# Optimization experiments

Measured on AMD Instinct MI355X. Metric: run time of the kernel, lower is better.

Reference implementation:

```python
import jax, jax.numpy as jnp
import numpy as np

HEADS = 8
LOCAL_ATTN_CTX = 64  # local_attn_ctx
BLOCKSIZE = 32       # only used for divisibility assert in original


def _strided_transpose(x, local_attn_ctx):
    # [n, t, e] -> group seq into (bT_ctx, local) blocks and transpose them
    n, t, e = x.shape
    bT_ctx = t // local_attn_ctx
    x = x.reshape(n, bT_ctx, local_attn_ctx, e)
    x = jnp.transpose(x, (0, 2, 1, 3))
    return x.reshape(n, t, e)


def setup_inputs() -> dict:
    key = jax.random.key(0)
    kq, kk, kv = jax.random.split(key, 3)
    shape = (4, 4096, 512)  # [batch, n_ctx, embd]
    return {
        "q": jax.random.normal(kq, shape, dtype=jnp.float32),
        "k": jax.random.normal(kk, shape, dtype=jnp.float32),
        "v": jax.random.normal(kv, shape, dtype=jnp.float32),
    }


def reference(q, k, v):
    n_ctx = q.shape[1]
    bT_ctx = n_ctx // LOCAL_ATTN_CTX
    assert bT_ctx % BLOCKSIZE == 0
    # strided permutation of the sequence axis
    qs = _strided_transpose(q, LOCAL_ATTN_CTX)
    ks = _strided_transpose(k, LOCAL_ATTN_CTX)
    vs = _strided_transpose(v, LOCAL_ATTN_CTX)
    n_state = q.shape[-1] // HEADS
    scale = np.float32(1.0 / np.sqrt(n_state))
    # full attention over the permuted sequence (as in the torch impl)
    w = jnp.einsum('nte,nse->nts', qs, ks)          # [n, t, t]
    w = jax.nn.softmax(w * scale, axis=-1)
    a = jnp.einsum('nts,nse->nte', w, vs)           # [n, t, e]
    # inverse strided regrouping
    n, t, e = a.shape
    a = a.reshape(n, LOCAL_ATTN_CTX, bT_ctx, e)
    a = jnp.transpose(a, (0, 2, 1, 3))
    return a.reshape(n, t, e)
```

## Files before the change

### kernel.cpp

```cpp
#include <hip/hip_runtime.h>


typedef _Float16 half8 __attribute__((ext_vector_type(8)));
typedef float f32x16 __attribute__((ext_vector_type(16)));
typedef float f32x4v __attribute__((ext_vector_type(4)));

#define B 4
#define S 4096
#define D 512
#define QT 64
#define NT 64
#define NELEM (B * S * D)

#define QSCALE 0.18033688011112042f
#define M0 20.0f

__global__ __launch_bounds__(256) void cvt(const float* __restrict__ k,
                                           const float* __restrict__ v,
                                           _Float16* __restrict__ k16,
                                           _Float16* __restrict__ v16) {
  __shared__ half8 tile[32][65];
  const int tid = threadIdx.x;
  int bx = blockIdx.x;
  if (bx < 512) {
    const int b = bx >> 7;
    const int t0 = (bx & 127) * 32;
#pragma unroll
    for (int p = 0; p < 8; ++p) {
      const int tl = p * 4 + (tid >> 6);
      const int dcl = tid & 63;
      const float* src = k + ((size_t)(b * S + t0 + tl) * D) + dcl * 8;
      f32x4v x = *(const f32x4v*)src;
      f32x4v y = *(const f32x4v*)(src + 4);
      half8 h;
      h[0] = (_Float16)x[0]; h[1] = (_Float16)x[1]; h[2] = (_Float16)x[2]; h[3] = (_Float16)x[3];
      h[4] = (_Float16)y[0]; h[5] = (_Float16)y[1]; h[6] = (_Float16)y[2]; h[7] = (_Float16)y[3];
      tile[tl][dcl] = h;
    }
    __syncthreads();
#pragma unroll
    for (int p = 0; p < 8; ++p) {
      const int dcw = p * 8 + (tid >> 5);
      const int tw = tid & 31;
      ((half8*)k16)[(size_t)(b * 64 + dcw) * S + t0 + tw] = tile[tw][dcw];
    }
  } else {
    bx -= 512;
    const int i = bx * 256 + tid;
    const int dq = i & 127;
    const int bt8 = i >> 7;
    const int b = bt8 >> 9, t8 = bt8 & 511;
    const float* src = v + ((size_t)(b * S + t8 * 8) * D) + dq * 4;
    f32x4v r[8];
#pragma unroll
    for (int j = 0; j < 8; ++j) r[j] = *(const f32x4v*)(src + (size_t)j * D);
    half8* dst = (half8*)v16 + ((size_t)bt8 * 512 + dq * 4);
#pragma unroll
    for (int c = 0; c < 4; ++c) {
      half8 h;
#pragma unroll
      for (int j = 0; j < 8; ++j) h[j] = (_Float16)r[j][c];
      dst[c] = h;
    }
  }
}

#define PBUF_H 5120
#define PBUF_OFF 0
#define SRED_OFF (2 * PBUF_H * 2)
#define LBUF_OFF (SRED_OFF + 16384)
#define SMEM_SZ  (LBUF_OFF + 512)

__global__ __launch_bounds__(1024, 4)
__attribute__((amdgpu_waves_per_eu(4, 4)))
void attn(const float* __restrict__ q,
          const _Float16* __restrict__ k16,
          const _Float16* __restrict__ v16,
          float* __restrict__ out) {
  __shared__ __align__(16) char smem[SMEM_SZ];
  _Float16* Pbuf = (_Float16*)(smem + PBUF_OFF);
  float*    Sred = (float*)(smem + SRED_OFF);
  float*    Lbuf = (float*)(smem + LBUF_OFF);

  const int tid = threadIdx.x;
  const int w = tid >> 6, lane = tid & 63;
  const int m32 = lane & 31, hi = lane >> 5;

  const int bx = blockIdx.x;
  const int xc = bx & 7, rr0 = bx >> 3;
  const int b = xc >> 1;
  const int qt = ((xc & 1) << 5) + rr0;

  if (w < 8) {
    const int rg = w & 1, kh = (w >> 1) & 1, dh = (w >> 2) & 1;
    const int qrow0 = qt * QT + rg * 32;

    const _Float16* kb = k16 + ((size_t)(b * 64 + dh * 32 + hi) * S + kh * 32 + m32) * 8;
    half8 kg[2][2];
#pragma unroll
    for (int i = 0; i < 2; ++i)
      kg[0][i] = *(const half8*)(kb + (size_t)i * (S * 16));

    half8 qf[16];
    {
      const float* qb = q + ((size_t)(b * S + qrow0 + m32) * D) + dh * 256 + hi * 8;
#pragma unroll
      for (int ks = 0; ks < 16; ++ks) {
        f32x4v x = *(const f32x4v*)(qb + ks * 16);
        f32x4v y = *(const f32x4v*)(qb + ks * 16 + 4);
        half8 h;
        h[0] = (_Float16)(x[0] * QSCALE); h[1] = (_Float16)(x[1] * QSCALE);
        h[2] = (_Float16)(x[2] * QSCALE); h[3] = (_Float16)(x[3] * QSCALE);
        h[4] = (_Float16)(y[0] * QSCALE); h[5] = (_Float16)(y[1] * QSCALE);
        h[6] = (_Float16)(y[2] * QSCALE); h[7] = (_Float16)(y[3] * QSCALE);
        qf[ks] = h;
      }
    }
    float* sredq = Sred + (kh * 2 + rg) * 1024 + lane * 4;

    if (dh == 1) {
      for (int t = 0; t <= NT; ++t) {
        asm volatile("" ::: "memory");
        __builtin_amdgcn_s_barrier();
        asm volatile("" ::: "memory");
        if (t == NT) break;
        f32x16 sa = {};
#pragma unroll
        for (int g = 0; g < 8; ++g) {
          if (g < 7) {
#pragma unroll
            for (int i = 0; i < 2; ++i)
              kg[(g + 1) & 1][i] = *(const half8*)(kb + (size_t)((g + 1) * 2 + i) * (S * 16) +
                                                   (size_t)t * 512);
          } else if (t + 1 < NT) {
#pragma unroll
            for (int i = 0; i < 2; ++i)
              kg[0][i] = *(const half8*)(kb + (size_t)i * (S * 16) + (size_t)(t + 1) * 512);
          }
          __builtin_amdgcn_s_setprio(1);
          sa = __builtin_amdgcn_mfma_f32_32x32x16_f16(qf[g * 2], kg[g & 1][0], sa, 0, 0, 0);
          sa = __builtin_amdgcn_mfma_f32_32x32x16_f16(qf[g * 2 + 1], kg[g & 1][1], sa, 0, 0, 0);
          __builtin_amdgcn_s_setprio(0);
        }
#pragma unroll
        for (int rq = 0; rq < 4; ++rq) {
          f32x4v x = {sa[rq * 4 + 0], sa[rq * 4 + 1], sa[rq * 4 + 2], sa[rq * 4 + 3]};
          *(f32x4v*)(sredq + rq * 256) = x;
        }
        asm volatile("s_waitcnt lgkmcnt(0)" ::: "memory");
        __builtin_amdgcn_s_barrier();
        asm volatile("" ::: "memory");
      }
      asm volatile("" ::: "memory");
      __builtin_amdgcn_s_barrier();
    } else {
      float lacc[16];
#pragma unroll
      for (int r = 0; r < 16; ++r) lacc[r] = 0.f;

      for (int t = 0; t <= NT; ++t) {
        asm volatile("s_waitcnt lgkmcnt(0)" ::: "memory");
        __builtin_amdgcn_s_barrier();
        asm volatile("" ::: "memory");
        if (t == NT) break;
        f32x16 sa = {};
#pragma unroll
        for (int g = 0; g < 8; ++g) {
          if (g < 7) {
#pragma unroll
            for (int i = 0; i < 2; ++i)
              kg[(g + 1) & 1][i] = *(const half8*)(kb + (size_t)((g + 1) * 2 + i) * (S * 16) +
                                                   (size_t)t * 512);
          } else if (t + 1 < NT) {
#pragma unroll
            for (int i = 0; i < 2; ++i)
              kg[0][i] = *(const half8*)(kb + (size_t)i * (S * 16) + (size_t)(t + 1) * 512);
          }
          __builtin_amdgcn_s_setprio(1);
          sa = __builtin_amdgcn_mfma_f32_32x32x16_f16(qf[g * 2], kg[g & 1][0], sa, 0, 0, 0);
          sa = __builtin_amdgcn_mfma_f32_32x32x16_f16(qf[g * 2 + 1], kg[g & 1][1], sa, 0, 0, 0);
          __builtin_amdgcn_s_setprio(0);
        }
        asm volatile("" ::: "memory");
        __builtin_amdgcn_s_barrier();
        asm volatile("" ::: "memory");
        _Float16* pq = &Pbuf[(t & 1) * PBUF_H + (kh * 2 + rg) * 1280];
#pragma unroll
        for (int rq = 0; rq < 4; ++rq) {
          f32x4v x = *(const f32x4v*)(sredq + rq * 256);
#pragma unroll
          for (int c = 0; c < 4; ++c) {
            const int r = rq * 4 + c;
            float p = __builtin_amdgcn_exp2f(fminf((sa[r] + x[c]) - M0, 15.0f));
            lacc[r] += p;
            const int row = c + 8 * rq + 4 * hi;
            pq[row * 40 + m32] = (_Float16)p;
          }
        }
      }

#pragma unroll
      for (int r = 0; r < 16; ++r) {
        float vv = lacc[r];
        vv += __shfl_xor(vv, 1);  vv += __shfl_xor(vv, 2);
        vv += __shfl_xor(vv, 4);  vv += __shfl_xor(vv, 8);
        vv += __shfl_xor(vv, 16);
        lacc[r] = vv;
      }
      if (m32 == 0) {
#pragma unroll
        for (int r = 0; r < 16; ++r) {
          const int row = (r & 3) + 8 * (r >> 2) + 4 * hi;
          Lbuf[kh * 64 + rg * 32 + row] = lacc[r];
        }
      }
      asm volatile("s_waitcnt lgkmcnt(0)" ::: "memory");
      __builtin_amdgcn_s_barrier();
    }
  } else {
    const int j = w - 8;
    f32x16 o[2][2];
#pragma unroll
    for (int rt = 0; rt < 2; ++rt)
#pragma unroll
      for (int dn = 0; dn < 2; ++dn) o[rt][dn] = (f32x16){};

    half8 vf[2][2], pf[2][4];
    const _Float16* vb0 = v16 + ((size_t)(b * 512 + hi) * 512 + j * 64 + m32) * 8;
#pragma unroll
    for (int dn = 0; dn < 2; ++dn)
      vf[0][dn] = *(const half8*)(vb0 + dn * 256);

    for (int t = 0; t <= NT; ++t) {
      asm volatile("" ::: "memory");
      __builtin_amdgcn_s_barrier();
      asm volatile("" ::: "memory");
      if (t > 0) {
        const _Float16* pb = &Pbuf[((t - 1) & 1) * PBUF_H];
#pragma unroll
        for (int rt = 0; rt < 2; ++rt)
#pragma unroll
          for (int ks = 0; ks < 4; ++ks)
            pf[rt][ks] = *(const half8*)(pb + ((ks >> 1) * 2 + rt) * 1280 + m32 * 40 +
                                         (ks & 1) * 16 + hi * 8);
      }
      if (t < NT) {
        asm volatile("" ::: "memory");
        __builtin_amdgcn_s_barrier();
        asm volatile("" ::: "memory");
      }
      if (t > 0) {
        const int u = t - 1;
        const _Float16* vb = vb0 + (size_t)u * 32768;
#pragma unroll
        for (int ks = 0; ks < 4; ++ks) {
          if (ks < 3) {
#pragma unroll
            for (int dn = 0; dn < 2; ++dn)
              vf[(ks + 1) & 1][dn] = *(const half8*)(vb + (size_t)(ks + 1) * 8192 + dn * 256);
          } else if (u + 1 < NT) {
#pragma unroll
            for (int dn = 0; dn < 2; ++dn)
              vf[0][dn] = *(const half8*)(vb + (size_t)32768 + dn * 256);
          }
          __builtin_amdgcn_s_setprio(1);
#pragma unroll
          for (int rt = 0; rt < 2; ++rt)
#pragma unroll
            for (int dn = 0; dn < 2; ++dn)
              o[rt][dn] = __builtin_amdgcn_mfma_f32_32x32x16_f16(pf[rt][ks], vf[ks & 1][dn],
                                                                 o[rt][dn], 0, 0, 0);
          __builtin_amdgcn_s_setprio(0);
        }
      }
    }

    asm volatile("" ::: "memory");
    __builtin_amdgcn_s_barrier();
    asm volatile("" ::: "memory");
    float* ob = out + (size_t)(b * S + qt * QT) * D + j * 64;
#pragma unroll
    for (int rt = 0; rt < 2; ++rt)
#pragma unroll
      for (int r = 0; r < 16; ++r) {
        const int row = rt * 32 + (r & 3) + 8 * (r >> 2) + 4 * hi;
        const float lt = Lbuf[row] + Lbuf[64 + row];
        const float inv = 1.0f / lt;
#pragma unroll
        for (int dn = 0; dn < 2; ++dn)
          ob[(size_t)row * D + dn * 32 + m32] = o[rt][dn][r] * inv;
      }
  }
}

extern "C" void kernel_launch(void* const* d_in, const int* in_sizes, int n_in,
                              void* d_out, int out_size, void* d_ws, size_t ws_size,
                              hipStream_t stream) {
  const float* q = (const float*)d_in[0];
  const float* k = (const float*)d_in[1];
  const float* v = (const float*)d_in[2];
  float* out = (float*)d_out;

  _Float16* k16 = (_Float16*)d_ws;
  _Float16* v16 = k16 + NELEM;

  cvt<<<1536, 256, 0, stream>>>(k, v, k16, v16);
  attn<<<256, 1024, 0, stream>>>(q, k16, v16, out);
}
```

Measured before the change: 300.5 us.

## Stage shared K tiles in LDS via async global-to-LDS loads, deepen V prefetch

The QK waves now cooperatively load most of each K tile straight into a double-buffered LDS region using global_load_lds. Each wave then reads its MFMA B-operands from LDS instead of every wave issuing redundant global loads, and the last two K chunks are still read from global into registers. The PV waves prefetch V in two half-tile batches of register fragments instead of one fragment per step. This cuts duplicated global traffic across waves but grows the LDS footprint by about 112KB, which may lower occupancy, and adds a vmcnt(0) wait before every barrier.

```diff
diff --git a/kernel.cpp b/kernel.cpp
--- a/kernel.cpp
+++ b/kernel.cpp
@@ -65,9 +65,11 @@
   }
 }
 
+#define KBUF_HALF 28672
+#define KBUF_OFF 0
 #define PBUF_H 5120
-#define PBUF_OFF 0
-#define SRED_OFF (2 * PBUF_H * 2)
+#define PBUF_OFF (2 * KBUF_HALF * 2)
+#define SRED_OFF (PBUF_OFF + 2 * PBUF_H * 2)
 #define LBUF_OFF (SRED_OFF + 16384)
 #define SMEM_SZ  (LBUF_OFF + 512)
 
@@ -78,6 +80,7 @@
           const _Float16* __restrict__ v16,
           float* __restrict__ out) {
   __shared__ __align__(16) char smem[SMEM_SZ];
+  _Float16* Kbuf = (_Float16*)(smem + KBUF_OFF);
   _Float16* Pbuf = (_Float16*)(smem + PBUF_OFF);
   float*    Sred = (float*)(smem + SRED_OFF);
   float*    Lbuf = (float*)(smem + LBUF_OFF);
@@ -95,11 +98,19 @@
     const int rg = w & 1, kh = (w >> 1) & 1, dh = (w >> 2) & 1;
     const int qrow0 = qt * QT + rg * 32;
 
-    const _Float16* kb = k16 + ((size_t)(b * 64 + dh * 32 + hi) * S + kh * 32 + m32) * 8;
-    half8 kg[2][2];
-#pragma unroll
-    for (int i = 0; i < 2; ++i)
-      kg[0][i] = *(const half8*)(kb + (size_t)i * (S * 16));
+    const int dc0 = w * 7 + (w >= 4 ? 4 : 0);
+    const int sdc0 = w * 7;
+#pragma unroll
+    for (int i = 0; i < 7; ++i) {
+      const _Float16* g = k16 + ((size_t)(b * 64 + dc0 + i) * S + lane) * 8;
+      __builtin_amdgcn_global_load_lds(
+          (const __attribute__((address_space(1))) void*)g,
+          (__attribute__((address_space(3))) void*)&Kbuf[(sdc0 + i) * 512],
+          16, 0, 0);
+    }
+
+    const _Float16* kds = Kbuf + (size_t)(dh * 28 + hi) * 512 + (kh * 32 + m32) * 8;
+    const _Float16* krb = k16 + ((size_t)(b * 64 + dh * 32 + 28 + hi) * S + kh * 32 + m32) * 8;
 
     half8 qf[16];
     {
@@ -120,28 +131,34 @@
 
     if (dh == 1) {
       for (int t = 0; t <= NT; ++t) {
-        asm volatile("" ::: "memory");
+        asm volatile("s_waitcnt vmcnt(0) lgkmcnt(0)" ::: "memory");
         __builtin_amdgcn_s_barrier();
         asm volatile("" ::: "memory");
         if (t == NT) break;
+        half8 kr0 = *(const half8*)(krb + (size_t)t * 512);
+        half8 kr1 = *(const half8*)(krb + (size_t)(S * 16) + (size_t)t * 512);
+        if (t + 1 < NT) {
+#pragma unroll
+          for (int i = 0; i < 7; ++i) {
+            const _Float16* g = k16 + ((size_t)(b * 64 + dc0 + i) * S + (t + 1) * 64 + lane) * 8;
+            __builtin_amdgcn_global_load_lds(
+                (const __attribute__((address_space(1))) void*)g,
+                (__attribute__((address_space(3))) void*)
+                    &Kbuf[((t + 1) & 1) * KBUF_HALF + (sdc0 + i) * 512],
+                16, 0, 0);
+          }
+        }
         f32x16 sa = {};
-#pragma unroll
-        for (int g = 0; g < 8; ++g) {
-          if (g < 7) {
-#pragma unroll
-            for (int i = 0; i < 2; ++i)
-              kg[(g + 1) & 1][i] = *(const half8*)(kb + (size_t)((g + 1) * 2 + i) * (S * 16) +
-                                                   (size_t)t * 512);
-          } else if (t + 1 < NT) {
-#pragma unroll
-            for (int i = 0; i < 2; ++i)
-              kg[0][i] = *(const half8*)(kb + (size_t)i * (S * 16) + (size_t)(t + 1) * 512);
-          }
-          __builtin_amdgcn_s_setprio(1);
-          sa = __builtin_amdgcn_mfma_f32_32x32x16_f16(qf[g * 2], kg[g & 1][0], sa, 0, 0, 0);
-          sa = __builtin_amdgcn_mfma_f32_32x32x16_f16(qf[g * 2 + 1], kg[g & 1][1], sa, 0, 0, 0);
-          __builtin_amdgcn_s_setprio(0);
-        }
+        const _Float16* kb2 = kds + (t & 1) * KBUF_HALF;
+        __builtin_amdgcn_s_setprio(1);
+#pragma unroll
+        for (int ks = 0; ks < 14; ++ks) {
+          half8 bf = *(const half8*)(kb2 + ks * 1024);
+          sa = __builtin_amdgcn_mfma_f32_32x32x16_f16(qf[ks], bf, sa, 0, 0, 0);
+        }
+        sa = __builtin_amdgcn_mfma_f32_32x32x16_f16(qf[14], kr0, sa, 0, 0, 0);
+        sa = __builtin_amdgcn_mfma_f32_32x32x16_f16(qf[15], kr1, sa, 0, 0, 0);
+        __builtin_amdgcn_s_setprio(0);
 #pragma unroll
         for (int rq = 0; rq < 4; ++rq) {
           f32x4v x = {sa[rq * 4 + 0], sa[rq * 4 + 1], sa[rq * 4 + 2], sa[rq * 4 + 3]};
@@ -159,28 +176,34 @@
       for (int r = 0; r < 16; ++r) lacc[r] = 0.f;
 
       for (int t = 0; t <= NT; ++t) {
-        asm volatile("s_waitcnt lgkmcnt(0)" ::: "memory");
+        asm volatile("s_waitcnt vmcnt(0) lgkmcnt(0)" ::: "memory");
         __builtin_amdgcn_s_barrier();
         asm volatile("" ::: "memory");
         if (t == NT) break;
+        half8 kr0 = *(const half8*)(krb + (size_t)t * 512);
+        half8 kr1 = *(const half8*)(krb + (size_t)(S * 16) + (size_t)t * 512);
+        if (t + 1 < NT) {
+#pragma unroll
+          for (int i = 0; i < 7; ++i) {
+            const _Float16* g = k16 + ((size_t)(b * 64 + dc0 + i) * S + (t + 1) * 64 + lane) * 8;
+            __builtin_amdgcn_global_load_lds(
+                (const __attribute__((address_space(1))) void*)g,
+                (__attribute__((address_space(3))) void*)
+                    &Kbuf[((t + 1) & 1) * KBUF_HALF + (sdc0 + i) * 512],
+                16, 0, 0);
+          }
+        }
         f32x16 sa = {};
-#pragma unroll
-        for (int g = 0; g < 8; ++g) {
-          if (g < 7) {
-#pragma unroll
-            for (int i = 0; i < 2; ++i)
-              kg[(g + 1) & 1][i] = *(const half8*)(kb + (size_t)((g + 1) * 2 + i) * (S * 16) +
-                                                   (size_t)t * 512);
-          } else if (t + 1 < NT) {
-#pragma unroll
-            for (int i = 0; i < 2; ++i)
-              kg[0][i] = *(const half8*)(kb + (size_t)i * (S * 16) + (size_t)(t + 1) * 512);
-          }
-          __builtin_amdgcn_s_setprio(1);
-          sa = __builtin_amdgcn_mfma_f32_32x32x16_f16(qf[g * 2], kg[g & 1][0], sa, 0, 0, 0);
-          sa = __builtin_amdgcn_mfma_f32_32x32x16_f16(qf[g * 2 + 1], kg[g & 1][1], sa, 0, 0, 0);
-          __builtin_amdgcn_s_setprio(0);
-        }
+        const _Float16* kb2 = kds + (t & 1) * KBUF_HALF;
+        __builtin_amdgcn_s_setprio(1);
+#pragma unroll
+        for (int ks = 0; ks < 14; ++ks) {
+          half8 bf = *(const half8*)(kb2 + ks * 1024);
+          sa = __builtin_amdgcn_mfma_f32_32x32x16_f16(qf[ks], bf, sa, 0, 0, 0);
+        }
+        sa = __builtin_amdgcn_mfma_f32_32x32x16_f16(qf[14], kr0, sa, 0, 0, 0);
+        sa = __builtin_amdgcn_mfma_f32_32x32x16_f16(qf[15], kr1, sa, 0, 0, 0);
+        __builtin_amdgcn_s_setprio(0);
         asm volatile("" ::: "memory");
         __builtin_amdgcn_s_barrier();
         asm volatile("" ::: "memory");
@@ -225,17 +248,21 @@
 #pragma unroll
       for (int dn = 0; dn < 2; ++dn) o[rt][dn] = (f32x16){};
 
-    half8 vf[2][2], pf[2][4];
+    half8 vf[2][2][2];
+    half8 pf[2][4];
     const _Float16* vb0 = v16 + ((size_t)(b * 512 + hi) * 512 + j * 64 + m32) * 8;
-#pragma unroll
-    for (int dn = 0; dn < 2; ++dn)
-      vf[0][dn] = *(const half8*)(vb0 + dn * 256);
 
     for (int t = 0; t <= NT; ++t) {
       asm volatile("" ::: "memory");
       __builtin_amdgcn_s_barrier();
       asm volatile("" ::: "memory");
-      if (t > 0) {
+      if (t == 0) {
+#pragma unroll
+        for (int kk = 0; kk < 2; ++kk)
+#pragma unroll
+          for (int dn = 0; dn < 2; ++dn)
+            vf[0][kk][dn] = *(const half8*)(vb0 + kk * 8192 + dn * 256);
+      } else {
         const _Float16* pb = &Pbuf[((t - 1) & 1) * PBUF_H];
 #pragma unroll
         for (int rt = 0; rt < 2; ++rt)
@@ -253,25 +280,37 @@
         const int u = t - 1;
         const _Float16* vb = vb0 + (size_t)u * 32768;
 #pragma unroll
-        for (int ks = 0; ks < 4; ++ks) {
-          if (ks < 3) {
+        for (int kk = 0; kk < 2; ++kk)
+#pragma unroll
+          for (int dn = 0; dn < 2; ++dn)
+            vf[1][kk][dn] = *(const half8*)(vb + (size_t)(2 + kk) * 8192 + dn * 256);
+        __builtin_amdgcn_s_setprio(1);
+#pragma unroll
+        for (int kk = 0; kk < 2; ++kk)
+#pragma unroll
+          for (int rt = 0; rt < 2; ++rt)
 #pragma unroll
             for (int dn = 0; dn < 2; ++dn)
-              vf[(ks + 1) & 1][dn] = *(const half8*)(vb + (size_t)(ks + 1) * 8192 + dn * 256);
-          } else if (u + 1 < NT) {
+              o[rt][dn] = __builtin_amdgcn_mfma_f32_32x32x16_f16(pf[rt][kk], vf[0][kk][dn],
+                                                                 o[rt][dn], 0, 0, 0);
+        __builtin_amdgcn_s_setprio(0);
+        if (u + 1 < NT) {
+#pragma unroll
+          for (int kk = 0; kk < 2; ++kk)
 #pragma unroll
             for (int dn = 0; dn < 2; ++dn)
-              vf[0][dn] = *(const half8*)(vb + (size_t)32768 + dn * 256);
-          }
-          __builtin_amdgcn_s_setprio(1);
+              vf[0][kk][dn] = *(const half8*)(vb + (size_t)32768 + (size_t)kk * 8192 + dn * 256);
+        }
+        __builtin_amdgcn_s_setprio(1);
+#pragma unroll
+        for (int kk = 0; kk < 2; ++kk)
 #pragma unroll
           for (int rt = 0; rt < 2; ++rt)
 #pragma unroll
             for (int dn = 0; dn < 2; ++dn)
-              o[rt][dn] = __builtin_amdgcn_mfma_f32_32x32x16_f16(pf[rt][ks], vf[ks & 1][dn],
+              o[rt][dn] = __builtin_amdgcn_mfma_f32_32x32x16_f16(pf[rt][2 + kk], vf[1][kk][dn],
                                                                  o[rt][dn], 0, 0, 0);
-          __builtin_amdgcn_s_setprio(0);
-        }
+        __builtin_amdgcn_s_setprio(0);
       }
     }
 
```

New measurement: 302.9 us. About the same (+0.8%).

## Stage V tiles through LDS via async global_load_lds in PV waves

Applied to the files above, without the earlier changes.

The PV-consumer waves now prefetch each V tile directly into a per-wave LDS buffer with global_load_lds, replacing direct global loads into registers. Fragments are then read from LDS, and the next tile's async load is issued after the last LDS read of the current tile. The aim is to hide global latency and reduce VGPR pressure. In exchange it adds 64KB of LDS, which may lower occupancy below the requested 4 waves per EU, and it adds a vmcnt(0) wait on every iteration.

```diff
diff --git a/kernel.cpp b/kernel.cpp
--- a/kernel.cpp
+++ b/kernel.cpp
@@ -69,7 +69,8 @@
 #define PBUF_OFF 0
 #define SRED_OFF (2 * PBUF_H * 2)
 #define LBUF_OFF (SRED_OFF + 16384)
-#define SMEM_SZ  (LBUF_OFF + 512)
+#define VBUF_OFF (LBUF_OFF + 512)
+#define SMEM_SZ  (VBUF_OFF + 8 * 8192)
 
 __global__ __launch_bounds__(1024, 4)
 __attribute__((amdgpu_waves_per_eu(4, 4)))
@@ -219,6 +220,7 @@
     }
   } else {
     const int j = w - 8;
+    _Float16* Vw = (_Float16*)(smem + VBUF_OFF) + (size_t)(w - 8) * 4096;
     f32x16 o[2][2];
 #pragma unroll
     for (int rt = 0; rt < 2; ++rt)
@@ -226,10 +228,12 @@
       for (int dn = 0; dn < 2; ++dn) o[rt][dn] = (f32x16){};
 
     half8 vf[2][2], pf[2][4];
-    const _Float16* vb0 = v16 + ((size_t)(b * 512 + hi) * 512 + j * 64 + m32) * 8;
-#pragma unroll
-    for (int dn = 0; dn < 2; ++dn)
-      vf[0][dn] = *(const half8*)(vb0 + dn * 256);
+    const _Float16* vsrc = v16 + ((size_t)(b * 512) * 512 + j * 64 + lane) * 8;
+#pragma unroll
+    for (int i = 0; i < 8; ++i)
+      __builtin_amdgcn_global_load_lds(
+          (const __attribute__((address_space(1))) void*)(vsrc + (size_t)i * 4096),
+          (__attribute__((address_space(3))) void*)&Vw[i * 512], 16, 0, 0);
 
     for (int t = 0; t <= NT; ++t) {
       asm volatile("" ::: "memory");
@@ -251,17 +255,27 @@
       }
       if (t > 0) {
         const int u = t - 1;
-        const _Float16* vb = vb0 + (size_t)u * 32768;
+        asm volatile("s_waitcnt vmcnt(0)" ::: "memory");
+#pragma unroll
+        for (int dn = 0; dn < 2; ++dn)
+          vf[0][dn] = *(const half8*)(Vw + ((hi) * 64 + dn * 32 + m32) * 8);
 #pragma unroll
         for (int ks = 0; ks < 4; ++ks) {
           if (ks < 3) {
 #pragma unroll
             for (int dn = 0; dn < 2; ++dn)
-              vf[(ks + 1) & 1][dn] = *(const half8*)(vb + (size_t)(ks + 1) * 8192 + dn * 256);
-          } else if (u + 1 < NT) {
-#pragma unroll
-            for (int dn = 0; dn < 2; ++dn)
-              vf[0][dn] = *(const half8*)(vb + (size_t)32768 + dn * 256);
+              vf[(ks + 1) & 1][dn] =
+                  *(const half8*)(Vw + (((ks + 1) * 2 + hi) * 64 + dn * 32 + m32) * 8);
+          } else {
+            asm volatile("s_waitcnt lgkmcnt(0)" ::: "memory");
+            if (u + 1 < NT) {
+#pragma unroll
+              for (int i = 0; i < 8; ++i)
+                __builtin_amdgcn_global_load_lds(
+                    (const __attribute__((address_space(1))) void*)
+                        (vsrc + (size_t)((u + 1) * 8 + i) * 4096),
+                    (__attribute__((address_space(3))) void*)&Vw[i * 512], 16, 0, 0);
+            }
           }
           __builtin_amdgcn_s_setprio(1);
 #pragma unroll
```

After: 298.6 us. Within noise of the previous version (-0.6%).
